# Optimization experiments

Hardware: AMD Instinct MI355X
Metric: run time of the kernel (lower is better)

The kernel has to match this reference:

```python
import jax, jax.numpy as jnp
import numpy as np
from jax import lax

B, S, H, W = 16, 5, 64, 64
D, DS, DEPTH, EXPAND, NC = 128, 16, 2, 2, 2


def _ln(x, w, b, eps=1e-5):
    m = x.mean(-1, keepdims=True)
    v = ((x - m) ** 2).mean(-1, keepdims=True)
    return (x - m) / jnp.sqrt(v + eps) * w + b


def _conv2d(x, w, b, stride, pad):
    y = lax.conv_general_dilated(x, w, (stride, stride), [(pad, pad), (pad, pad)],
                                 dimension_numbers=('NCHW', 'OIHW', 'NCHW'))
    return y + b[None, :, None, None]


def _convT2d(x, w, b):
    # torch ConvTranspose2d(k=4, s=2, p=1); w: (Cin, Cout, 4, 4)
    k = jnp.transpose(w[:, :, ::-1, ::-1], (1, 0, 2, 3))
    y = lax.conv_general_dilated(x, k, (1, 1), [(2, 2), (2, 2)], lhs_dilation=(2, 2),
                                 dimension_numbers=('NCHW', 'OIHW', 'NCHW'))
    return y + b[None, :, None, None]


def _dwconv1d(x, w, b):
    # x: [B, L, D]; torch depthwise Conv1d k=4 pad=3 then truncate to L == left-pad 3
    y = lax.conv_general_dilated(x.transpose(0, 2, 1), w, (1,), [(3, 0)],
                                 feature_group_count=w.shape[0],
                                 dimension_numbers=('NCH', 'OIH', 'NCH'))
    return (y + b[None, :, None]).transpose(0, 2, 1)


def _selective_scan(x, ln_w, ln_b, in_w, in_b, x_w, x_b, A_log, Dm, out_w, out_b):
    xn = _ln(x, ln_w, ln_b)
    xz = xn @ in_w.T + in_b
    xp, z = jnp.split(xz, 2, axis=-1)
    xp = jax.nn.silu(xp)
    z = jax.nn.sigmoid(z)
    u = xp @ x_w.T + x_b                        # [B, L, DS]
    a = jnp.exp(-jnp.exp(A_log))[0, 0]          # [DS] decay factor exp(A), A = -exp(A_log)

    def step(h, u_t):
        h = a * h + u_t
        return h, h

    _, hs = lax.scan(step, jnp.zeros((x.shape[0], DS), x.dtype), u.transpose(1, 0, 2))
    hs = hs.transpose(1, 0, 2)                  # [B, L, DS]
    y = (hs @ Dm) * z
    y = y @ out_w.T + out_b                     # dropout is identity at inference
    return x + y


def setup_inputs() -> dict:
    key = jax.random.key(0)
    ks = iter(jax.random.split(key, 64))

    def nrm(shape, scale=0.02):
        return (jax.random.normal(next(ks), shape) * scale).astype(jnp.float32)

    d, ds, hw = D, DS, H * W
    return {
        'x': jax.random.normal(next(ks), (B, S, H, W), dtype=jnp.float32),
        'emb_w': nrm((d, 1, 3, 3), 0.1), 'emb_b': jnp.zeros((d,), jnp.float32),
        'pos_embed': nrm((hw, d)), 'time_embed': nrm((S, d)),
        'blk_ln1_w': jnp.ones((DEPTH, d), jnp.float32), 'blk_ln1_b': jnp.zeros((DEPTH, d), jnp.float32),
        'blk_conv_w': nrm((DEPTH, d, 1, 4), 0.2), 'blk_conv_b': jnp.zeros((DEPTH, d), jnp.float32),
        'blk_sln_w': jnp.ones((DEPTH, d), jnp.float32), 'blk_sln_b': jnp.zeros((DEPTH, d), jnp.float32),
        'blk_A_log': nrm((DEPTH, 1, 1, ds), 0.5),
        'blk_D': nrm((DEPTH, ds, d), 0.1),
        'blk_in_w': nrm((DEPTH, 2 * d, d), 0.05), 'blk_in_b': jnp.zeros((DEPTH, 2 * d), jnp.float32),
        'blk_x_w': nrm((DEPTH, ds, d), 0.05), 'blk_x_b': jnp.zeros((DEPTH, ds), jnp.float32),
        'blk_out_w': nrm((DEPTH, d, d), 0.05), 'blk_out_b': jnp.zeros((DEPTH, d), jnp.float32),
        'blk_ln2_w': jnp.ones((DEPTH, d), jnp.float32), 'blk_ln2_b': jnp.zeros((DEPTH, d), jnp.float32),
        'blk_mlp_w1': nrm((DEPTH, EXPAND * d, d), 0.05), 'blk_mlp_b1': jnp.zeros((DEPTH, EXPAND * d), jnp.float32),
        'blk_mlp_w2': nrm((DEPTH, d, EXPAND * d), 0.05), 'blk_mlp_b2': jnp.zeros((DEPTH, d), jnp.float32),
        'down1_w': nrm((d, d, 3, 3), 0.05), 'down1_b': jnp.zeros((d,), jnp.float32),
        'down2_w': nrm((2 * d, d, 3, 3), 0.05), 'down2_b': jnp.zeros((2 * d,), jnp.float32),
        'bott_w': nrm((2 * d, 2 * d, 3, 3), 0.05), 'bott_b': jnp.zeros((2 * d,), jnp.float32),
        'up1_w': nrm((2 * d, d, 4, 4), 0.05), 'up1_b': jnp.zeros((d,), jnp.float32),
        'up2_w': nrm((2 * d, d, 4, 4), 0.05), 'up2_b': jnp.zeros((d,), jnp.float32),
        'final_w': nrm((NC, 2 * d, 1, 1), 0.05), 'final_b': jnp.zeros((NC,), jnp.float32),
    }


def reference(x, emb_w, emb_b, pos_embed, time_embed,
              blk_ln1_w, blk_ln1_b, blk_conv_w, blk_conv_b,
              blk_sln_w, blk_sln_b, blk_A_log, blk_D,
              blk_in_w, blk_in_b, blk_x_w, blk_x_b, blk_out_w, blk_out_b,
              blk_ln2_w, blk_ln2_b, blk_mlp_w1, blk_mlp_b1, blk_mlp_w2, blk_mlp_b2,
              down1_w, down1_b, down2_w, down2_b, bott_w, bott_b,
              up1_w, up1_b, up2_w, up2_b, final_w, final_b):
    b, s, h, w = x.shape
    # embed all frames at once (linear combination weights: 0.5 each, last frame 1.0)
    e = _conv2d(x.reshape(b * s, 1, h, w), emb_w, emb_b, 1, 1)      # [B*S, D, H, W]
    e = e.reshape(b, s, D, h * w).transpose(0, 1, 3, 2)              # [B, S, HW, D]
    e = e + pos_embed[None, None] + time_embed[:s][None, :, None, :]
    wts = jnp.where(jnp.arange(s) == s - 1, 1.0, 0.5).astype(x.dtype)
    emb = jnp.einsum('bsld,s->bld', e, wts)                          # [B, HW, D]
    for i in range(DEPTH):
        xn = _ln(emb, blk_ln1_w[i], blk_ln1_b[i])
        emb = emb + _dwconv1d(xn, blk_conv_w[i], blk_conv_b[i])
        emb = _selective_scan(emb, blk_sln_w[i], blk_sln_b[i], blk_in_w[i], blk_in_b[i],
                              blk_x_w[i], blk_x_b[i], blk_A_log[i], blk_D[i],
                              blk_out_w[i], blk_out_b[i])
        m = _ln(emb, blk_ln2_w[i], blk_ln2_b[i])
        m = jax.nn.gelu(m @ blk_mlp_w1[i].T + blk_mlp_b1[i], approximate=False)
        emb = emb + (m @ blk_mlp_w2[i].T + blk_mlp_b2[i])
    sp = emb.transpose(0, 2, 1).reshape(b, D, h, w)
    x1 = jax.nn.relu(_conv2d(sp, down1_w, down1_b, 2, 1))
    x2 = jax.nn.relu(_conv2d(x1, down2_w, down2_b, 2, 1))
    x2 = jax.nn.relu(_conv2d(x2, bott_w, bott_b, 1, 1))
    u1 = jax.nn.relu(_convT2d(x2, up1_w, up1_b))
    u1 = jnp.concatenate([u1, x1], axis=1)
    u2 = jax.nn.relu(_convT2d(u1, up2_w, up2_b))
    u2 = jnp.concatenate([u2, sp], axis=1)
    return _conv2d(u2, final_w, final_b, 1, 0)
```

## Files before the change

kernel.cpp:

```cpp
#include <hip/hip_runtime.h>
#include <cmath>

namespace {
constexpr int Bn = 16, Ln = 4096, Dn = 128, DSn = 16;
constexpr int Mtok = Bn * Ln;
constexpr int SLS = 138;
}

typedef short bfx8 __attribute__((ext_vector_type(8)));
typedef float f32x4 __attribute__((ext_vector_type(4)));

static __device__ __forceinline__ ushort f2bf(float f) {
  union { float f; unsigned u; } v; v.f = f;
  unsigned r = v.u + 0x7fff + ((v.u >> 16) & 1);
  return (ushort)(r >> 16);
}
static __device__ __forceinline__ float bf2f(ushort u) {
  union { unsigned u; float f; } v; v.u = ((unsigned)u) << 16;
  return v.f;
}

__global__ void k_prep(const float* __restrict__ inw, const float* __restrict__ outw,
                       const float* __restrict__ m1, const float* __restrict__ m2,
                       const float* __restrict__ xw, const float* __restrict__ cw,
// ... 131 lines not shown
    r8[e] = (short)f2bf((nv[e] - m) * rs * sw[d] + sb[d]);
  }
  *(bfx8*)(xn2 + (size_t)tok * 128 + d0) = r8;
}

__global__ __launch_bounds__(256) void k_gemm_xz(
    const ushort* __restrict__ A, const ushort* __restrict__ W, const float* __restrict__ bias,
    ushort* __restrict__ Zu, const ushort* __restrict__ xw, const float* __restrict__ xb,
    float* __restrict__ UT) {
  __shared__ ushort sl[128 * SLS];
  const int t = threadIdx.x;
  const int l = t & 63, wv = t >> 6;
  const int l15 = l & 15, q = l >> 4;
  const int wm = wv >> 1, wn = wv & 1;
  const int m0 = blockIdx.x * 128 + wm * 64;
  const int n0 = blockIdx.y * 128 + wn * 64;
  f32x4 acc[4][4] = {};
  const ushort* Ab = A + (size_t)(m0 + l15) * 128 + q * 8;
  const ushort* Wb = W + (size_t)(n0 + l15) * 128 + q * 8;
#pragma unroll
  for (int k0 = 0; k0 < 128; k0 += 32) {
    bfx8 a[4], b[4];
#pragma unroll
    for (int mf = 0; mf < 4; mf++) a[mf] = *(const bfx8*)(Ab + (size_t)mf * 16 * 128 + k0);
#pragma unroll
    for (int nf = 0; nf < 4; nf++) b[nf] = *(const bfx8*)(Wb + (size_t)nf * 16 * 128 + k0);
#pragma unroll
    for (int mf = 0; mf < 4; mf++)
#pragma unroll
      for (int nf = 0; nf < 4; nf++)
        acc[mf][nf] = __builtin_amdgcn_mfma_f32_16x16x32_bf16(a[mf], b[nf], acc[mf][nf], 0, 0, 0);
  }
  if (blockIdx.y == 1) {
#pragma unroll
    for (int mf = 0; mf < 4; mf++)
#pragma unroll
      for (int nf = 0; nf < 4; nf++) {
        const int col = n0 + nf * 16 + l15;
        const float bb = bias[col];
#pragma unroll
        for (int r = 0; r < 4; r++) {
          const int row = m0 + mf * 16 + q * 4 + r;
          float v = acc[mf][nf][r] + bb;
          Zu[(size_t)row * 128 + col - 128] = f2bf(1.f / (1.f + expf(-v)));
        }
      }
    return;
  }
#pragma unroll
  for (int mf = 0; mf < 4; mf++)
#pragma unroll
    for (int nf = 0; nf < 4; nf++) {
      const int col = wn * 64 + nf * 16 + l15;
      const float bb = bias[col];
#pragma unroll
      for (int r = 0; r < 4; r++) {
        const int rowl = wm * 64 + mf * 16 + q * 4 + r;
        float v = acc[mf][nf][r] + bb;
        sl[rowl * SLS + col] = f2bf(v / (1.f + expf(-v)));
      }
    }
  __syncthreads();
  f32x4 pu[2] = {};
#pragma unroll
  for (int k0 = 0; k0 < 128; k0 += 32) {
    bfx8 bx_ = *(const bfx8*)(xw + l15 * 128 + k0 + q * 8);
#pragma unroll
    for (int mi = 0; mi < 2; mi++) {
      bfx8 a2 = *(const bfx8*)&sl[(wv * 32 + mi * 16 + l15) * SLS + k0 + q * 8];
      pu[mi] = __builtin_amdgcn_mfma_f32_16x16x32_bf16(a2, bx_, pu[mi], 0, 0, 0);
    }
  }
  const float ub = xb[l15];
#pragma unroll
  for (int mi = 0; mi < 2; mi++)
#pragma unroll
    for (int r = 0; r < 4; r++) {
      int token = blockIdx.x * 128 + wv * 32 + mi * 16 + q * 4 + r;
      int b = token >> 12, ll = token & 4095;
      UT[((size_t)(b * 16 + l15)) * 4096 + ll] = pu[mi][r] + ub;
    }
}

__global__ __launch_bounds__(256) void k_gemm_om(
    const ushort* __restrict__ A, const ushort* __restrict__ W1, const float* __restrict__ b1,
    float* __restrict__ emb, const float* __restrict__ lw, const float* __restrict__ lb,
    const ushort* __restrict__ W2, const float* __restrict__ b2, ushort* __restrict__ MH) {
  __shared__ ushort sl[128 * SLS];
  __shared__ float red[2][128][2];
  const int t = threadIdx.x;
  const int l = t & 63, wv = t >> 6;
  const int l15 = l & 15, q = l >> 4;
  const int wm = wv >> 1, wn = wv & 1;
  const int m0 = blockIdx.x * 128 + wm * 64;
  const int n0 = wn * 64;
  {
    f32x4 acc[4][4] = {};
    const ushort* Ab = A + (size_t)(m0 + l15) * 128 + q * 8;
    const ushort* Wb = W1 + (size_t)(n0 + l15) * 128 + q * 8;
#pragma unroll
    for (int k0 = 0; k0 < 128; k0 += 32) {
      bfx8 a[4], b[4];
#pragma unroll
      for (int mf = 0; mf < 4; mf++) a[mf] = *(const bfx8*)(Ab + (size_t)mf * 16 * 128 + k0);
#pragma unroll
      for (int nf = 0; nf < 4; nf++) b[nf] = *(const bfx8*)(Wb + (size_t)nf * 16 * 128 + k0);
#pragma unroll
      for (int mf = 0; mf < 4; mf++)
#pragma unroll
        for (int nf = 0; nf < 4; nf++)
          acc[mf][nf] = __builtin_amdgcn_mfma_f32_16x16x32_bf16(a[mf], b[nf], acc[mf][nf], 0, 0, 0);
    }
    float sv[4][4], qv[4][4];
#pragma unroll
    for (int mf = 0; mf < 4; mf++)
#pragma unroll
      for (int r = 0; r < 4; r++) { sv[mf][r] = 0.f; qv[mf][r] = 0.f; }
#pragma unroll
    for (int mf = 0; mf < 4; mf++)
#pragma unroll
      for (int nf = 0; nf < 4; nf++) {
        const int col = n0 + nf * 16 + l15;
        const float bb = b1[col];
#pragma unroll
        for (int r = 0; r < 4; r++) {
          const int row = m0 + mf * 16 + q * 4 + r;
          float v = acc[mf][nf][r] + bb + emb[(size_t)row * 128 + col];
          acc[mf][nf][r] = v;
          sv[mf][r] += v; qv[mf][r] += v * v;
        }
      }
#pragma unroll
    for (int mf = 0; mf < 4; mf++)
#pragma unroll
      for (int r = 0; r < 4; r++) {
#pragma unroll
        for (int off = 1; off < 16; off <<= 1) {
          sv[mf][r] += __shfl_xor(sv[mf][r], off);
          qv[mf][r] += __shfl_xor(qv[mf][r], off);
        }
        if (l15 == 0) {
          int rowl = wm * 64 + mf * 16 + q * 4 + r;
          red[0][rowl][wn] = sv[mf][r];
          red[1][rowl][wn] = qv[mf][r];
        }
      }
    __syncthreads();
#pragma unroll
    for (int mf = 0; mf < 4; mf++)
#pragma unroll
      for (int r = 0; r < 4; r++) {
        const int rowl = wm * 64 + mf * 16 + q * 4 + r;
        const int row = blockIdx.x * 128 + rowl;
        float ts = red[0][rowl][0] + red[0][rowl][1];
        float tq = red[1][rowl][0] + red[1][rowl][1];
        float mm = ts * (1.f / 128.f);
        float var = tq * (1.f / 128.f) - mm * mm;
        float rs = rsqrtf(var + 1e-5f);
#pragma unroll
        for (int nf = 0; nf < 4; nf++) {
          const int col = n0 + nf * 16 + l15;
          float v = acc[mf][nf][r];
          emb[(size_t)row * 128 + col] = v;
          sl[rowl * SLS + col] = f2bf((v - mm) * rs * lw[col] + lb[col]);
        }
      }
  }
  __syncthreads();
#pragma unroll
  for (int p = 0; p < 2; p++) {
    f32x4 acc2[2][8] = {};
#pragma unroll
    for (int k0 = 0; k0 < 128; k0 += 32) {
      bfx8 a2[2];
#pragma unroll
      for (int mi = 0; mi < 2; mi++)
        a2[mi] = *(const bfx8*)&sl[(wv * 32 + mi * 16 + l15) * SLS + k0 + q * 8];
#pragma unroll
      for (int nf = 0; nf < 8; nf++) {
        bfx8 b2v = *(const bfx8*)(W2 + (size_t)(p * 128 + nf * 16 + l15) * 128 + k0 + q * 8);
#pragma unroll
        for (int mi = 0; mi < 2; mi++)
          acc2[mi][nf] = __builtin_amdgcn_mfma_f32_16x16x32_bf16(a2[mi], b2v, acc2[mi][nf], 0, 0, 0);
      }
    }
#pragma unroll
    for (int mi = 0; mi < 2; mi++)
#pragma unroll
      for (int nf = 0; nf < 8; nf++) {
        const int col = p * 128 + nf * 16 + l15;
        const float bb = b2[col];
#pragma unroll
        for (int r = 0; r < 4; r++) {
          const int row = blockIdx.x * 128 + wv * 32 + mi * 16 + q * 4 + r;
          float v = acc2[mi][nf][r] + bb;
          MH[(size_t)row * 256 + col] = f2bf(0.5f * v * (1.f + erff(v * 0.7071067811865475f)));
        }
      }
  }
}

template <int MODE, int K>
__global__ __launch_bounds__(256) void k_mgemm(const ushort* __restrict__ A, const ushort* __restrict__ W,
                                               const float* __restrict__ bias, void* __restrict__ out2v,
                                               float* __restrict__ emb,
                                               const float* __restrict__ lw, const float* __restrict__ lb) {
  __shared__ float red[2][128][2];
  const int t = threadIdx.x;
  const int l = t & 63, wv = t >> 6;
  const int l15 = l & 15, q = l >> 4;
  const int wm = wv >> 1, wn = wv & 1;
  const int m0 = blockIdx.x * 128 + wm * 64;
  const int n0 = wn * 64;
  f32x4 acc[4][4] = {};
  const ushort* Ab = A + (size_t)(m0 + l15) * K + q * 8;
  const ushort* Wb = W + (size_t)(n0 + l15) * K + q * 8;
#pragma unroll
  for (int k0 = 0; k0 < K; k0 += 32) {
    bfx8 a[4], b[4];
#pragma unroll
    for (int mf = 0; mf < 4; mf++) a[mf] = *(const bfx8*)(Ab + (size_t)mf * 16 * K + k0);
#pragma unroll
    for (int nf = 0; nf < 4; nf++) b[nf] = *(const bfx8*)(Wb + (size_t)nf * 16 * K + k0);
#pragma unroll
    for (int mf = 0; mf < 4; mf++)
#pragma unroll
      for (int nf = 0; nf < 4; nf++)
        acc[mf][nf] = __builtin_amdgcn_mfma_f32_16x16x32_bf16(a[mf], b[nf], acc[mf][nf], 0, 0, 0);
  }
  float sv[4][4], qv[4][4];
#pragma unroll
  for (int mf = 0; mf < 4; mf++)
#pragma unroll
    for (int r = 0; r < 4; r++) { sv[mf][r] = 0.f; qv[mf][r] = 0.f; }
#pragma unroll
  for (int mf = 0; mf < 4; mf++)
#pragma unroll
    for (int nf = 0; nf < 4; nf++) {
      const int col = n0 + nf * 16 + l15;
      const float bb = bias[col];
#pragma unroll
      for (int r = 0; r < 4; r++) {
        const int row = m0 + mf * 16 + q * 4 + r;
        float v = acc[mf][nf][r] + bb + emb[(size_t)row * 128 + col];
        acc[mf][nf][r] = v;
        sv[mf][r] += v; qv[mf][r] += v * v;
      }
    }
  if constexpr (MODE == 5) {
#pragma unroll
    for (int mf = 0; mf < 4; mf++)
#pragma unroll
      for (int r = 0; r < 4; r++) {
#pragma unroll
        for (int off = 1; off < 16; off <<= 1) {
          sv[mf][r] += __shfl_xor(sv[mf][r], off);
          qv[mf][r] += __shfl_xor(qv[mf][r], off);
        }
        if (l15 == 0) {
          int rowl = wm * 64 + mf * 16 + q * 4 + r;
          red[0][rowl][wn] = sv[mf][r];
          red[1][rowl][wn] = qv[mf][r];
        }
      }
    __syncthreads();
  }
#pragma unroll
  for (int mf = 0; mf < 4; mf++)
#pragma unroll
    for (int r = 0; r < 4; r++) {
      const int rowl = wm * 64 + mf * 16 + q * 4 + r;
      const int row = blockIdx.x * 128 + rowl;
      float mm = 0.f, rs = 0.f;
      if constexpr (MODE == 5) {
        float ts = red[0][rowl][0] + red[0][rowl][1];
        float tq = red[1][rowl][0] + red[1][rowl][1];
        mm = ts * (1.f / 128.f);
        float var = tq * (1.f / 128.f) - mm * mm;
        rs = rsqrtf(var + 1e-5f);
      }
#pragma unroll
      for (int nf = 0; nf < 4; nf++) {
        const int col = n0 + nf * 16 + l15;
        float v = acc[mf][nf][r];
        emb[(size_t)row * 128 + col] = v;
        if constexpr (MODE == 5)
          ((ushort*)out2v)[(size_t)row * 128 + col] = f2bf((v - mm) * rs * lw[col] + lb[col]);
        else
          ((ushort*)out2v)[(size_t)row * 256 + 128 + col] = f2bf(v);
      }
    }
}

__global__ __launch_bounds__(64) void k_scan(const float* __restrict__ UT, float* __restrict__ HST,
                                             const float* __restrict__ A_log) {
  const int b = blockIdx.x >> 4, ds = blockIdx.x & 15;
  const int tid = threadIdx.x;
  const float a = expf(-expf(A_log[ds]));
  const float4* ut4 = (const float4*)(UT + ((size_t)(b * 16 + ds)) * 4096 + tid * 64);
  float r[64];
#pragma unroll
  for (int j4 = 0; j4 < 16; j4++) {
    float4 v = ut4[j4];
    r[j4 * 4 + 0] = v.x; r[j4 * 4 + 1] = v.y; r[j4 * 4 + 2] = v.z; r[j4 * 4 + 3] = v.w;
  }
  float h = 0.f;
#pragma unroll
  for (int j = 0; j < 64; j++) { h = a * h + r[j]; r[j] = h; }
  float a64 = a;
#pragma unroll
  for (int qq = 0; qq < 6; qq++) a64 *= a64;
  float Ac = a64, Bc = h;
#pragma unroll
  for (int off = 1; off < 64; off <<= 1) {
    float Ap = __shfl_up(Ac, off);
    float Bp = __shfl_up(Bc, off);
    if (tid >= off) { Bc = Ac * Bp + Bc; Ac = Ac * Ap; }
  }
  float carry = __shfl_up(Bc, 1);
  if (tid == 0) carry = 0.f;
  float p = a;
#pragma unroll
  for (int j = 0; j < 64; j++) { r[j] += p * carry; p *= a; }
  float4* hb4 = (float4*)(HST + ((size_t)(b * 16 + ds)) * 4096 + tid * 64);
#pragma unroll
  for (int j4 = 0; j4 < 16; j4++) {
    float4 v; v.x = r[j4 * 4 + 0]; v.y = r[j4 * 4 + 1]; v.z = r[j4 * 4 + 2]; v.w = r[j4 * 4 + 3];
    hb4[j4] = v;
  }
}

__global__ __launch_bounds__(256) void k_yb(const float* __restrict__ HST, const float* __restrict__ Dm_,
                                            const ushort* __restrict__ Z, ushort* __restrict__ Y) {
  const int m = blockIdx.x * 2 + (threadIdx.x >> 7);
  const int d = threadIdx.x & 127;
  const int b = m >> 12, l = m & 4095;
  const float* hb = HST + (size_t)b * 16 * Ln + l;
  float acc = 0.f;
#pragma unroll
  for (int s = 0; s < 16; s++) acc += hb[(size_t)s * Ln] * Dm_[s * 128 + d];
  const size_t o = (size_t)m * 128 + d;
  Y[o] = f2bf(acc * bf2f(Z[o]));
}

template <int MODE, int OTH, int OTW, int CIN, int WPB>
__global__ __launch_bounds__(WPB * 64) void k_cv(
    const ushort* __restrict__ in, ushort* __restrict__ out,
    const ushort* __restrict__ wt, const float* __restrict__ bias,
    int Hi, int Wi, int CP, int CO, int CPo, int COo, int Cout,
    int nsp, int nspx, long ibs, long obs) {
  constexpr int ITH = (MODE == 1) ? (2 * OTH + 1) : (OTH + 2);
  constexpr int ITW = (MODE == 1) ? (2 * OTW + 1) : (OTW + 2);
  constexpr int NPIX = ITH * ITW;
  constexpr int SPF = OTH * OTW / 16;
  constexpr int NTAPS = (MODE == 2) ? 4 : 9;
  constexpr int NCH = CIN / 32;
  __shared__ __attribute__((aligned(16))) ushort lds[NPIX * 40];
  const int t = threadIdx.x;
  const int w = t >> 6, l = t & 63;
  const int l15 = l & 15, q = l >> 4;
  const int b = blockIdx.z;
  const int py = (MODE == 2) ? ((int)blockIdx.y >> 1) : 0;
  const int px = (MODE == 2) ? ((int)blockIdx.y & 1) : 0;
  const int cb = blockIdx.x / nsp;
  const int spt = blockIdx.x - cb * nsp;
  const int spy = spt / nspx, spx = spt - spy * nspx;
  const int n0 = cb * (16 * WPB) + w * 16;
  const int y0 = spy * OTH, x0 = spx * OTW;
  const int gy0 = (MODE == 1) ? (2 * y0 - 1) : (y0 - 1);
  const int gx0 = (MODE == 1) ? (2 * x0 - 1) : (x0 - 1);
  const ushort* ib = in + (size_t)b * ibs;
  f32x4 acc[SPF] = {};
  int abase[SPF];
#pragma unroll
  for (int af = 0; af < SPF; af++) {
    int p = af * 16 + l15;
    int ty = p / OTW, tx = p % OTW;
    int sy = (MODE == 1) ? (2 * ty) : ty;
    int sx = (MODE == 1) ? (2 * tx) : tx;
    abase[af] = (sy * ITW + sx) * 40 + q * 8;
  }
  for (int c = 0; c < NCH; c++) {
    const int k0 = c * 32;
    __syncthreads();
    for (int idx = t; idx < NPIX * 4; idx += WPB * 64) {
      int pix = idx >> 2, qq = idx & 3;
      int sy = pix / ITW, sx = pix - sy * ITW;
      int gy = gy0 + sy, gx = gx0 + sx;
      bfx8 v = {0, 0, 0, 0, 0, 0, 0, 0};
      if ((unsigned)gy < (unsigned)Hi && (unsigned)gx < (unsigned)Wi)
        v = *(const bfx8*)(ib + (size_t)(gy * Wi + gx) * CP + CO + k0 + qq * 8);
      *(bfx8*)&lds[pix * 40 + qq * 8] = v;
    }
    __syncthreads();
#pragma unroll
    for (int tap = 0; tap < NTAPS; tap++) {
      const int dy = (MODE == 2) ? (tap >> 1) : (tap / 3);
      const int dx = (MODE == 2) ? (tap & 1) : (tap - (tap / 3) * 3);
      const int tapw = (MODE == 2) ? ((3 - py - 2 * dy) * 4 + (3 - px - 2 * dx)) : tap;
      const int toff = (MODE == 2) ? (((py + dy) * ITW + (px + dx)) * 40)
                                   : ((dy * ITW + dx) * 40);
      bfx8 bv = *(const bfx8*)(wt + ((size_t)tapw * Cout + n0 + l15) * CIN + k0 + q * 8);
#pragma unroll
      for (int af = 0; af < SPF; af++) {
        bfx8 av = *(const bfx8*)&lds[abase[af] + toff];
        acc[af] = __builtin_amdgcn_mfma_f32_16x16x32_bf16(av, bv, acc[af], 0, 0, 0);
      }
    }
  }
  const float bb = bias[n0 + l15];
  ushort* ob = out + (size_t)b * obs + COo + n0 + l15;
#pragma unroll
  for (int af = 0; af < SPF; af++) {
#pragma unroll
    for (int r = 0; r < 4; r++) {
      int p = af * 16 + q * 4 + r;
      int ty = p / OTW, tx = p % OTW;
      int oy, ox, Wo;
      if (MODE == 2) { oy = (y0 + ty) * 2 + py; ox = (x0 + tx) * 2 + px; Wo = Wi * 2; }
      else if (MODE == 1) { oy = y0 + ty; ox = x0 + tx; Wo = Wi / 2; }
      else { oy = y0 + ty; ox = x0 + tx; Wo = Wi; }
      ob[(size_t)(oy * Wo + ox) * CPo] = f2bf(fmaxf(acc[af][r] + bb, 0.f));
    }
  }
}

__global__ void k_final2(const ushort* __restrict__ in, const float* __restrict__ w,
                         const float* __restrict__ bias, float* __restrict__ out) {
  int i = blockIdx.x * 256 + threadIdx.x;
  int b = i >> 12, p = i & 4095;
  const ushort* row = in + (size_t)i * 256;
  float a0 = bias[0], a1 = bias[1];
  for (int c = 0; c < 256; c += 4) {
    ushort4 u = *(const ushort4*)(row + c);
    float4 w0 = *(const float4*)(w + c);
    float4 w1 = *(const float4*)(w + 256 + c);
    float f0 = bf2f(u.x), f1 = bf2f(u.y), f2 = bf2f(u.z), f3 = bf2f(u.w);
    a0 += f0 * w0.x + f1 * w0.y + f2 * w0.z + f3 * w0.w;
    a1 += f0 * w1.x + f1 * w1.y + f2 * w1.z + f3 * w1.w;
  }
  out[(size_t)b * 8192 + p] = a0;
  out[(size_t)b * 8192 + 4096 + p] = a1;
}

extern "C" void kernel_launch(void* const* d_in, const int* in_sizes, int n_in,
                              void* d_out, int out_size, void* d_ws, size_t ws_size,
                              hipStream_t stream) {
  (void)in_sizes; (void)n_in; (void)out_size; (void)ws_size;
  const float* x          = (const float*)d_in[0];
  const float* emb_w      = (const float*)d_in[1];
  const float* emb_b      = (const float*)d_in[2];
  const float* pos_embed  = (const float*)d_in[3];
  const float* time_embed = (const float*)d_in[4];
  const float* blk_ln1_w  = (const float*)d_in[5];
  const float* blk_ln1_b  = (const float*)d_in[6];
  const float* blk_conv_w = (const float*)d_in[7];
  const float* blk_conv_b = (const float*)d_in[8];
  const float* blk_sln_w  = (const float*)d_in[9];
  const float* blk_sln_b  = (const float*)d_in[10];
  const float* blk_A_log  = (const float*)d_in[11];
  const float* blk_D      = (const float*)d_in[12];
  const float* blk_in_w   = (const float*)d_in[13];
  const float* blk_in_b   = (const float*)d_in[14];
  const float* blk_x_w    = (const float*)d_in[15];
  const float* blk_x_b    = (const float*)d_in[16];
  const float* blk_out_w  = (const float*)d_in[17];
  const float* blk_out_b  = (const float*)d_in[18];
  const float* blk_ln2_w  = (const float*)d_in[19];
  const float* blk_ln2_b  = (const float*)d_in[20];
  const float* blk_mlp_w1 = (const float*)d_in[21];
  const float* blk_mlp_b1 = (const float*)d_in[22];
  const float* blk_mlp_w2 = (const float*)d_in[23];
  const float* blk_mlp_b2 = (const float*)d_in[24];
  const float* down1_w    = (const float*)d_in[25];
  const float* down1_b    = (const float*)d_in[26];
  const float* down2_w    = (const float*)d_in[27];
  const float* down2_b    = (const float*)d_in[28];
  const float* bott_w     = (const float*)d_in[29];
  const float* bott_b     = (const float*)d_in[30];
  const float* up1_w      = (const float*)d_in[31];
  const float* up1_b      = (const float*)d_in[32];
  const float* up2_w      = (const float*)d_in[33];
  const float* up2_b      = (const float*)d_in[34];
  const float* final_w    = (const float*)d_in[35];
  const float* final_b    = (const float*)d_in[36];

  float* ws = (float*)d_ws;
  constexpr size_t F = 1u << 20;
  float* EMB = ws;
  ushort* XN1 = (ushort*)(ws + 8 * F);
  ushort* XN2 = XN1 + 8 * F;
  ushort* MH  = (ushort*)(ws + 16 * F);
  ushort* Zu  = (ushort*)(ws + 24 * F);
  ushort* W3  = (ushort*)(ws + 28 * F);
  float* Ubuf = ws + 32 * F;
  float* HST  = ws + 33 * F;

  ushort* Wi  = W3;
  ushort* Wo  = W3 + 65536;
  ushort* Wm1 = W3 + 98304;
  ushort* Wm2 = W3 + 163840;
  ushort* Wx  = W3 + 229376;
  ushort* Wd1 = W3 + 233472;
  ushort* Wd2 = W3 + 380928;
  ushort* Wb9 = W3 + 675840;
  ushort* Wu1 = W3 + 1265664;
  ushort* Wu2 = W3 + 1789952;
  float*  CWT = (float*)(W3 + 2314240);

  k_prep<<<9044, 256, 0, stream>>>(blk_in_w, blk_out_w, blk_mlp_w1, blk_mlp_w2, blk_x_w,
                                   blk_conv_w, down1_w, down2_w, bott_w, up1_w, up2_w, W3, CWT);
  k_combine<<<256, 256, 0, stream>>>(x, Ubuf);
  k_embedln<<<8192, 256, 0, stream>>>(Ubuf, emb_w, emb_b, pos_embed, time_embed,
                                      blk_ln1_w, blk_ln1_b, EMB, XN1);

  ushort* U2C = MH;
  for (int i = 0; i < 2; i++) {
    k_fuse1<<<4096, 256, 0, stream>>>(XN1, EMB, XN2, CWT + i * 512, blk_conv_b + i * Dn,
                                      blk_sln_w + i * Dn, blk_sln_b + i * Dn);
    k_gemm_xz<<<dim3(512, 2), 256, 0, stream>>>(XN2, Wi + i * 32768, blk_in_b + i * 256,
                                                Zu, Wx + i * 2048, blk_x_b + i * DSn, Ubuf);
    k_scan<<<256, 64, 0, stream>>>(Ubuf, HST, blk_A_log + i * DSn);
    k_yb<<<32768, 256, 0, stream>>>(HST, blk_D + i * DSn * Dn, Zu, XN2);
    k_gemm_om<<<dim3(512, 1), 256, 0, stream>>>(XN2, Wo + i * 16384, blk_out_b + i * Dn,
                                                EMB, blk_ln2_w + i * Dn, blk_ln2_b + i * Dn,
                                                Wm1 + i * 32768, blk_mlp_b1 + i * 256, MH);
    if (i == 0)
      k_mgemm<5, 256><<<dim3(512, 1), 256, 0, stream>>>(MH, Wm2 + i * 32768, blk_mlp_b2 + i * Dn,
                                                        XN1, EMB, blk_ln1_w + Dn, blk_ln1_b + Dn);
    else
      k_mgemm<4, 256><<<dim3(512, 1), 256, 0, stream>>>(MH, Wm2 + i * 32768, blk_mlp_b2 + i * Dn,
                                                        U2C, EMB, nullptr, nullptr);
  }

  ushort* U1C = XN1;
  ushort* X2b = XN1 + 8388608;
  ushort* X3b = X2b + 1048576;

  k_cv<1, 8, 8, 128, 4><<<dim3(2 * 16, 1, 16), 256, 0, stream>>>(
      U2C, U1C, Wd1, down1_b, 64, 64, 256, 128, 256, 128, 128,
      16, 4, 64L * 64 * 256, 32L * 32 * 256);
  k_cv<1, 8, 8, 128, 2><<<dim3(8 * 4, 1, 16), 128, 0, stream>>>(
      U1C, X2b, Wd2, down2_b, 32, 32, 256, 128, 256, 0, 256,
      4, 2, 32L * 32 * 256, 16L * 16 * 256);
  k_cv<0, 8, 8, 256, 2><<<dim3(8 * 4, 1, 16), 128, 0, stream>>>(
      X2b, X3b, Wb9, bott_b, 16, 16, 256, 0, 256, 0, 256,
      4, 2, 16L * 16 * 256, 16L * 16 * 256);
  k_cv<2, 8, 16, 256, 2><<<dim3(4 * 2, 4, 16), 128, 0, stream>>>(
      X3b, U1C, Wu1, up1_b, 16, 16, 256, 0, 256, 0, 128,
      2, 1, 16L * 16 * 256, 32L * 32 * 256);
  k_cv<2, 16, 16, 256, 4><<<dim3(2 * 4, 4, 16), 256, 0, stream>>>(
      U1C, U2C, Wu2, up2_b, 32, 32, 256, 0, 256, 0, 128,
      4, 2, 32L * 32 * 256, 64L * 64 * 256);

  k_final2<<<256, 256, 0, stream>>>(U2C, final_w, final_b, (float*)d_out);
}
```

Baseline: 503.5 us.

## Fuse out-proj, LN2, MLP up and down GEMMs into one kernel; warp-parallel final conv

Merges the out-projection+LN2+MLP1 kernel with the MLP2 GEMM kernel. The GELU hidden activations are now staged through a second shared-memory tile in two 128-column halves, so the 256-wide MH intermediate is never written to or read back from global memory. The final 1x1 conv changes from one thread per pixel looping over 256 channels to one wavefront per pixel with a shuffle reduction, which gives more parallelism and coalesced loads. In exchange, shared memory per block roughly doubles and register pressure rises, which may reduce occupancy.

```diff
diff --git a/kernel.cpp b/kernel.cpp
--- a/kernel.cpp
+++ b/kernel.cpp
@@ -237,11 +237,15 @@
     }
 }
 
-__global__ __launch_bounds__(256) void k_gemm_om(
+template <int MODE>
+__global__ __launch_bounds__(256) void k_blk2(
     const ushort* __restrict__ A, const ushort* __restrict__ W1, const float* __restrict__ b1,
     float* __restrict__ emb, const float* __restrict__ lw, const float* __restrict__ lb,
-    const ushort* __restrict__ W2, const float* __restrict__ b2, ushort* __restrict__ MH) {
-  __shared__ ushort sl[128 * SLS];
+    const ushort* __restrict__ W2, const float* __restrict__ b2,
+    const ushort* __restrict__ W3m, const float* __restrict__ b3,
+    void* __restrict__ out2v, const float* __restrict__ lwn, const float* __restrict__ lbn) {
+  __shared__ ushort sl1[128 * SLS];
+  __shared__ ushort sl2[128 * SLS];
   __shared__ float red[2][128][2];
   const int t = threadIdx.x;
   const int l = t & 63, wv = t >> 6;
@@ -317,71 +321,102 @@
           const int col = n0 + nf * 16 + l15;
           float v = acc[mf][nf][r];
           emb[(size_t)row * 128 + col] = v;
-          sl[rowl * SLS + col] = f2bf((v - mm) * rs * lw[col] + lb[col]);
+          sl1[rowl * SLS + col] = f2bf((v - mm) * rs * lw[col] + lb[col]);
         }
       }
   }
   __syncthreads();
-#pragma unroll
-  for (int p = 0; p < 2; p++) {
-    f32x4 acc2[2][8] = {};
+  {
+    f32x4 g[2][8] = {};
 #pragma unroll
     for (int k0 = 0; k0 < 128; k0 += 32) {
       bfx8 a2[2];
 #pragma unroll
       for (int mi = 0; mi < 2; mi++)
-        a2[mi] = *(const bfx8*)&sl[(wv * 32 + mi * 16 + l15) * SLS + k0 + q * 8];
+        a2[mi] = *(const bfx8*)&sl1[(wv * 32 + mi * 16 + l15) * SLS + k0 + q * 8];
 #pragma unroll
       for (int nf = 0; nf < 8; nf++) {
-        bfx8 b2v = *(const bfx8*)(W2 + (size_t)(p * 128 + nf * 16 + l15) * 128 + k0 + q * 8);
+        bfx8 bv = *(const bfx8*)(W2 + (size_t)(nf * 16 + l15) * 128 + k0 + q * 8);
 #pragma unroll
         for (int mi = 0; mi < 2; mi++)
-          acc2[mi][nf] = __builtin_amdgcn_mfma_f32_16x16x32_bf16(a2[mi], b2v, acc2[mi][nf], 0, 0, 0);
+          g[mi][nf] = __builtin_amdgcn_mfma_f32_16x16x32_bf16(a2[mi], bv, g[mi][nf], 0, 0, 0);
       }
     }
 #pragma unroll
     for (int mi = 0; mi < 2; mi++)
 #pragma unroll
       for (int nf = 0; nf < 8; nf++) {
-        const int col = p * 128 + nf * 16 + l15;
+        const int col = nf * 16 + l15;
         const float bb = b2[col];
 #pragma unroll
         for (int r = 0; r < 4; r++) {
-          const int row = blockIdx.x * 128 + wv * 32 + mi * 16 + q * 4 + r;
-          float v = acc2[mi][nf][r] + bb;
-          MH[(size_t)row * 256 + col] = f2bf(0.5f * v * (1.f + erff(v * 0.7071067811865475f)));
-        }
-      }
-  }
-}
-
-template <int MODE, int K>
-__global__ __launch_bounds__(256) void k_mgemm(const ushort* __restrict__ A, const ushort* __restrict__ W,
-                                               const float* __restrict__ bias, void* __restrict__ out2v,
-                                               float* __restrict__ emb,
-                                               const float* __restrict__ lw, const float* __restrict__ lb) {
-  __shared__ float red[2][128][2];
-  const int t = threadIdx.x;
-  const int l = t & 63, wv = t >> 6;
-  const int l15 = l & 15, q = l >> 4;
-  const int wm = wv >> 1, wn = wv & 1;
-  const int m0 = blockIdx.x * 128 + wm * 64;
-  const int n0 = wn * 64;
-  f32x4 acc[4][4] = {};
-  const ushort* Ab = A + (size_t)(m0 + l15) * K + q * 8;
-  const ushort* Wb = W + (size_t)(n0 + l15) * K + q * 8;
-#pragma unroll
-  for (int k0 = 0; k0 < K; k0 += 32) {
+          const int rowl = wv * 32 + mi * 16 + q * 4 + r;
+          float v = g[mi][nf][r] + bb;
+          sl2[rowl * SLS + col] = f2bf(0.5f * v * (1.f + erff(v * 0.7071067811865475f)));
+        }
+      }
+  }
+  __syncthreads();
+  f32x4 g1[2][8] = {};
+#pragma unroll
+  for (int k0 = 0; k0 < 128; k0 += 32) {
+    bfx8 a2[2];
+#pragma unroll
+    for (int mi = 0; mi < 2; mi++)
+      a2[mi] = *(const bfx8*)&sl1[(wv * 32 + mi * 16 + l15) * SLS + k0 + q * 8];
+#pragma unroll
+    for (int nf = 0; nf < 8; nf++) {
+      bfx8 bv = *(const bfx8*)(W2 + (size_t)(128 + nf * 16 + l15) * 128 + k0 + q * 8);
+#pragma unroll
+      for (int mi = 0; mi < 2; mi++)
+        g1[mi][nf] = __builtin_amdgcn_mfma_f32_16x16x32_bf16(a2[mi], bv, g1[mi][nf], 0, 0, 0);
+    }
+  }
+  f32x4 acc3[4][4] = {};
+#pragma unroll
+  for (int k0 = 0; k0 < 128; k0 += 32) {
     bfx8 a[4], b[4];
 #pragma unroll
-    for (int mf = 0; mf < 4; mf++) a[mf] = *(const bfx8*)(Ab + (size_t)mf * 16 * K + k0);
-#pragma unroll
-    for (int nf = 0; nf < 4; nf++) b[nf] = *(const bfx8*)(Wb + (size_t)nf * 16 * K + k0);
+    for (int mf = 0; mf < 4; mf++)
+      a[mf] = *(const bfx8*)&sl2[(wm * 64 + mf * 16 + l15) * SLS + k0 + q * 8];
+#pragma unroll
+    for (int nf = 0; nf < 4; nf++)
+      b[nf] = *(const bfx8*)(W3m + (size_t)(n0 + nf * 16 + l15) * 256 + k0 + q * 8);
 #pragma unroll
     for (int mf = 0; mf < 4; mf++)
 #pragma unroll
       for (int nf = 0; nf < 4; nf++)
-        acc[mf][nf] = __builtin_amdgcn_mfma_f32_16x16x32_bf16(a[mf], b[nf], acc[mf][nf], 0, 0, 0);
+        acc3[mf][nf] = __builtin_amdgcn_mfma_f32_16x16x32_bf16(a[mf], b[nf], acc3[mf][nf], 0, 0, 0);
+  }
+  __syncthreads();
+#pragma unroll
+  for (int mi = 0; mi < 2; mi++)
+#pragma unroll
+    for (int nf = 0; nf < 8; nf++) {
+      const int col = nf * 16 + l15;
+      const float bb = b2[128 + col];
+#pragma unroll
+      for (int r = 0; r < 4; r++) {
+        const int rowl = wv * 32 + mi * 16 + q * 4 + r;
+        float v = g1[mi][nf][r] + bb;
+        sl2[rowl * SLS + col] = f2bf(0.5f * v * (1.f + erff(v * 0.7071067811865475f)));
+      }
+    }
+  __syncthreads();
+#pragma unroll
+  for (int k0 = 0; k0 < 128; k0 += 32) {
+    bfx8 a[4], b[4];
+#pragma unroll
+    for (int mf = 0; mf < 4; mf++)
+      a[mf] = *(const bfx8*)&sl2[(wm * 64 + mf * 16 + l15) * SLS + k0 + q * 8];
+#pragma unroll
+    for (int nf = 0; nf < 4; nf++)
+      b[nf] = *(const bfx8*)(W3m + (size_t)(n0 + nf * 16 + l15) * 256 + 128 + k0 + q * 8);
+#pragma unroll
+    for (int mf = 0; mf < 4; mf++)
+#pragma unroll
+      for (int nf = 0; nf < 4; nf++)
+        acc3[mf][nf] = __builtin_amdgcn_mfma_f32_16x16x32_bf16(a[mf], b[nf], acc3[mf][nf], 0, 0, 0);
   }
   float sv[4][4], qv[4][4];
 #pragma unroll
@@ -393,12 +428,12 @@
 #pragma unroll
     for (int nf = 0; nf < 4; nf++) {
       const int col = n0 + nf * 16 + l15;
-      const float bb = bias[col];
+      const float bb = b3[col];
 #pragma unroll
       for (int r = 0; r < 4; r++) {
         const int row = m0 + mf * 16 + q * 4 + r;
-        float v = acc[mf][nf][r] + bb + emb[(size_t)row * 128 + col];
-        acc[mf][nf][r] = v;
+        float v = acc3[mf][nf][r] + bb + emb[(size_t)row * 128 + col];
+        acc3[mf][nf][r] = v;
         sv[mf][r] += v; qv[mf][r] += v * v;
       }
     }
@@ -437,12 +472,13 @@
 #pragma unroll
       for (int nf = 0; nf < 4; nf++) {
         const int col = n0 + nf * 16 + l15;
-        float v = acc[mf][nf][r];
-        emb[(size_t)row * 128 + col] = v;
-        if constexpr (MODE == 5)
-          ((ushort*)out2v)[(size_t)row * 128 + col] = f2bf((v - mm) * rs * lw[col] + lb[col]);
-        else
+        float v = acc3[mf][nf][r];
+        if constexpr (MODE == 5) {
+          emb[(size_t)row * 128 + col] = v;
+          ((ushort*)out2v)[(size_t)row * 128 + col] = f2bf((v - mm) * rs * lwn[col] + lbn[col]);
+        } else {
           ((ushort*)out2v)[(size_t)row * 256 + 128 + col] = f2bf(v);
+        }
       }
     }
 }
@@ -580,22 +616,24 @@
   }
 }
 
-__global__ void k_final2(const ushort* __restrict__ in, const float* __restrict__ w,
-                         const float* __restrict__ bias, float* __restrict__ out) {
-  int i = blockIdx.x * 256 + threadIdx.x;
-  int b = i >> 12, p = i & 4095;
-  const ushort* row = in + (size_t)i * 256;
-  float a0 = bias[0], a1 = bias[1];
-  for (int c = 0; c < 256; c += 4) {
-    ushort4 u = *(const ushort4*)(row + c);
-    float4 w0 = *(const float4*)(w + c);
-    float4 w1 = *(const float4*)(w + 256 + c);
-    float f0 = bf2f(u.x), f1 = bf2f(u.y), f2 = bf2f(u.z), f3 = bf2f(u.w);
-    a0 += f0 * w0.x + f1 * w0.y + f2 * w0.z + f3 * w0.w;
-    a1 += f0 * w1.x + f1 * w1.y + f2 * w1.z + f3 * w1.w;
-  }
-  out[(size_t)b * 8192 + p] = a0;
-  out[(size_t)b * 8192 + 4096 + p] = a1;
+__global__ __launch_bounds__(256) void k_final3(const ushort* __restrict__ in, const float* __restrict__ w,
+                                                const float* __restrict__ bias, float* __restrict__ out) {
+  int wid = (blockIdx.x << 2) + (threadIdx.x >> 6);
+  int lane = threadIdx.x & 63;
+  const ushort* rp = in + (size_t)wid * 256 + lane * 4;
+  ushort4 u = *(const ushort4*)rp;
+  float f0 = bf2f(u.x), f1 = bf2f(u.y), f2 = bf2f(u.z), f3 = bf2f(u.w);
+  float4 w0 = *(const float4*)(w + lane * 4);
+  float4 w1 = *(const float4*)(w + 256 + lane * 4);
+  float a0 = f0 * w0.x + f1 * w0.y + f2 * w0.z + f3 * w0.w;
+  float a1 = f0 * w1.x + f1 * w1.y + f2 * w1.z + f3 * w1.w;
+#pragma unroll
+  for (int off = 32; off; off >>= 1) { a0 += __shfl_xor(a0, off); a1 += __shfl_xor(a1, off); }
+  if (lane == 0) {
+    int b = wid >> 12, p = wid & 4095;
+    out[(size_t)b * 8192 + p] = a0 + bias[0];
+    out[(size_t)b * 8192 + 4096 + p] = a1 + bias[1];
+  }
 }
 
 extern "C" void kernel_launch(void* const* d_in, const int* in_sizes, int n_in,
@@ -645,7 +683,7 @@
   float* EMB = ws;
   ushort* XN1 = (ushort*)(ws + 8 * F);
   ushort* XN2 = XN1 + 8 * F;
-  ushort* MH  = (ushort*)(ws + 16 * F);
+  ushort* U2C = (ushort*)(ws + 16 * F);
   ushort* Zu  = (ushort*)(ws + 24 * F);
   ushort* W3  = (ushort*)(ws + 28 * F);
   float* Ubuf = ws + 32 * F;
@@ -669,7 +707,6 @@
   k_embedln<<<8192, 256, 0, stream>>>(Ubuf, emb_w, emb_b, pos_embed, time_embed,
                                       blk_ln1_w, blk_ln1_b, EMB, XN1);
 
-  ushort* U2C = MH;
   for (int i = 0; i < 2; i++) {
     k_fuse1<<<4096, 256, 0, stream>>>(XN1, EMB, XN2, CWT + i * 512, blk_conv_b + i * Dn,
                                       blk_sln_w + i * Dn, blk_sln_b + i * Dn);
@@ -677,15 +714,18 @@
                                                 Zu, Wx + i * 2048, blk_x_b + i * DSn, Ubuf);
     k_scan<<<256, 64, 0, stream>>>(Ubuf, HST, blk_A_log + i * DSn);
     k_yb<<<32768, 256, 0, stream>>>(HST, blk_D + i * DSn * Dn, Zu, XN2);
-    k_gemm_om<<<dim3(512, 1), 256, 0, stream>>>(XN2, Wo + i * 16384, blk_out_b + i * Dn,
-                                                EMB, blk_ln2_w + i * Dn, blk_ln2_b + i * Dn,
-                                                Wm1 + i * 32768, blk_mlp_b1 + i * 256, MH);
     if (i == 0)
-      k_mgemm<5, 256><<<dim3(512, 1), 256, 0, stream>>>(MH, Wm2 + i * 32768, blk_mlp_b2 + i * Dn,
-                                                        XN1, EMB, blk_ln1_w + Dn, blk_ln1_b + Dn);
+      k_blk2<5><<<512, 256, 0, stream>>>(XN2, Wo + i * 16384, blk_out_b + i * Dn,
+                                         EMB, blk_ln2_w + i * Dn, blk_ln2_b + i * Dn,
+                                         Wm1 + i * 32768, blk_mlp_b1 + i * 256,
+                                         Wm2 + i * 32768, blk_mlp_b2 + i * Dn,
+                                         XN1, blk_ln1_w + Dn, blk_ln1_b + Dn);
     else
-      k_mgemm<4, 256><<<dim3(512, 1), 256, 0, stream>>>(MH, Wm2 + i * 32768, blk_mlp_b2 + i * Dn,
-                                                        U2C, EMB, nullptr, nullptr);
+      k_blk2<4><<<512, 256, 0, stream>>>(XN2, Wo + i * 16384, blk_out_b + i * Dn,
+                                         EMB, blk_ln2_w + i * Dn, blk_ln2_b + i * Dn,
+                                         Wm1 + i * 32768, blk_mlp_b1 + i * 256,
+                                         Wm2 + i * 32768, blk_mlp_b2 + i * Dn,
+                                         U2C, nullptr, nullptr);
   }
 
   ushort* U1C = XN1;
@@ -708,5 +748,5 @@
       U1C, U2C, Wu2, up2_b, 32, 32, 256, 0, 256, 0, 128,
       4, 2, 32L * 32 * 256, 64L * 64 * 256);
 
-  k_final2<<<256, 256, 0, stream>>>(U2C, final_w, final_b, (float*)d_out);
-}
+  k_final3<<<16384, 256, 0, stream>>>(U2C, final_w, final_b, (float*)d_out);
+}
```

Result: slower. 529.3 us (+5.1%).

## Halve GEMM row tiles to double grid and parallelize final 1x1 conv per wave

Applied to the files above, without the earlier changes.

The fused out-proj/LN/MLP1 kernel and the MLP2 kernel now process 64 token rows per block instead of 128. Each wave holds half the accumulators and the launch uses twice as many blocks, which raises occupancy and gives better spread across CUs on 65536 tokens. The final 1x1 conv now assigns one wavefront per pixel with a shuffle reduction, replacing one thread per pixel that walked 256 channels serially. The cost is that each weight tile is reloaded by twice as many blocks, and an extra barrier is added in the MODE 4 path.

```diff
diff --git a/kernel.cpp b/kernel.cpp
--- a/kernel.cpp
+++ b/kernel.cpp
@@ -241,52 +241,52 @@
     const ushort* __restrict__ A, const ushort* __restrict__ W1, const float* __restrict__ b1,
     float* __restrict__ emb, const float* __restrict__ lw, const float* __restrict__ lb,
     const ushort* __restrict__ W2, const float* __restrict__ b2, ushort* __restrict__ MH) {
-  __shared__ ushort sl[128 * SLS];
-  __shared__ float red[2][128][2];
+  __shared__ ushort sl1[64 * SLS];
+  __shared__ float red[2][64][2];
   const int t = threadIdx.x;
   const int l = t & 63, wv = t >> 6;
   const int l15 = l & 15, q = l >> 4;
   const int wm = wv >> 1, wn = wv & 1;
-  const int m0 = blockIdx.x * 128 + wm * 64;
+  const int m0 = blockIdx.x * 64;
   const int n0 = wn * 64;
   {
-    f32x4 acc[4][4] = {};
-    const ushort* Ab = A + (size_t)(m0 + l15) * 128 + q * 8;
+    f32x4 acc[2][4] = {};
+    const ushort* Ab = A + (size_t)(m0 + wm * 32 + l15) * 128 + q * 8;
     const ushort* Wb = W1 + (size_t)(n0 + l15) * 128 + q * 8;
 #pragma unroll
     for (int k0 = 0; k0 < 128; k0 += 32) {
-      bfx8 a[4], b[4];
-#pragma unroll
-      for (int mf = 0; mf < 4; mf++) a[mf] = *(const bfx8*)(Ab + (size_t)mf * 16 * 128 + k0);
+      bfx8 a[2], b[4];
+#pragma unroll
+      for (int mf = 0; mf < 2; mf++) a[mf] = *(const bfx8*)(Ab + (size_t)mf * 16 * 128 + k0);
 #pragma unroll
       for (int nf = 0; nf < 4; nf++) b[nf] = *(const bfx8*)(Wb + (size_t)nf * 16 * 128 + k0);
 #pragma unroll
-      for (int mf = 0; mf < 4; mf++)
+      for (int mf = 0; mf < 2; mf++)
 #pragma unroll
         for (int nf = 0; nf < 4; nf++)
           acc[mf][nf] = __builtin_amdgcn_mfma_f32_16x16x32_bf16(a[mf], b[nf], acc[mf][nf], 0, 0, 0);
     }
-    float sv[4][4], qv[4][4];
-#pragma unroll
-    for (int mf = 0; mf < 4; mf++)
+    float sv[2][4], qv[2][4];
+#pragma unroll
+    for (int mf = 0; mf < 2; mf++)
 #pragma unroll
       for (int r = 0; r < 4; r++) { sv[mf][r] = 0.f; qv[mf][r] = 0.f; }
 #pragma unroll
-    for (int mf = 0; mf < 4; mf++)
+    for (int mf = 0; mf < 2; mf++)
 #pragma unroll
       for (int nf = 0; nf < 4; nf++) {
         const int col = n0 + nf * 16 + l15;
         const float bb = b1[col];
 #pragma unroll
         for (int r = 0; r < 4; r++) {
-          const int row = m0 + mf * 16 + q * 4 + r;
+          const int row = m0 + wm * 32 + mf * 16 + q * 4 + r;
           float v = acc[mf][nf][r] + bb + emb[(size_t)row * 128 + col];
           acc[mf][nf][r] = v;
           sv[mf][r] += v; qv[mf][r] += v * v;
         }
       }
 #pragma unroll
-    for (int mf = 0; mf < 4; mf++)
+    for (int mf = 0; mf < 2; mf++)
 #pragma unroll
       for (int r = 0; r < 4; r++) {
 #pragma unroll
@@ -295,18 +295,18 @@
           qv[mf][r] += __shfl_xor(qv[mf][r], off);
         }
         if (l15 == 0) {
-          int rowl = wm * 64 + mf * 16 + q * 4 + r;
+          int rowl = wm * 32 + mf * 16 + q * 4 + r;
           red[0][rowl][wn] = sv[mf][r];
           red[1][rowl][wn] = qv[mf][r];
         }
       }
     __syncthreads();
 #pragma unroll
-    for (int mf = 0; mf < 4; mf++)
+    for (int mf = 0; mf < 2; mf++)
 #pragma unroll
       for (int r = 0; r < 4; r++) {
-        const int rowl = wm * 64 + mf * 16 + q * 4 + r;
-        const int row = blockIdx.x * 128 + rowl;
+        const int rowl = wm * 32 + mf * 16 + q * 4 + r;
+        const int row = m0 + rowl;
         float ts = red[0][rowl][0] + red[0][rowl][1];
         float tq = red[1][rowl][0] + red[1][rowl][1];
         float mm = ts * (1.f / 128.f);
@@ -317,42 +317,41 @@
           const int col = n0 + nf * 16 + l15;
           float v = acc[mf][nf][r];
           emb[(size_t)row * 128 + col] = v;
-          sl[rowl * SLS + col] = f2bf((v - mm) * rs * lw[col] + lb[col]);
+          sl1[rowl * SLS + col] = f2bf((v - mm) * rs * lw[col] + lb[col]);
         }
       }
   }
   __syncthreads();
-#pragma unroll
-  for (int p = 0; p < 2; p++) {
-    f32x4 acc2[2][8] = {};
-#pragma unroll
-    for (int k0 = 0; k0 < 128; k0 += 32) {
-      bfx8 a2[2];
+  const int rw0 = (wv & 1) * 32;
+  const int cw0 = (wv >> 1) * 128;
+  f32x4 acc2[2][8] = {};
+#pragma unroll
+  for (int k0 = 0; k0 < 128; k0 += 32) {
+    bfx8 a2[2];
+#pragma unroll
+    for (int mi = 0; mi < 2; mi++)
+      a2[mi] = *(const bfx8*)&sl1[(rw0 + mi * 16 + l15) * SLS + k0 + q * 8];
+#pragma unroll
+    for (int nf = 0; nf < 8; nf++) {
+      bfx8 b2v = *(const bfx8*)(W2 + (size_t)(cw0 + nf * 16 + l15) * 128 + k0 + q * 8);
 #pragma unroll
       for (int mi = 0; mi < 2; mi++)
-        a2[mi] = *(const bfx8*)&sl[(wv * 32 + mi * 16 + l15) * SLS + k0 + q * 8];
-#pragma unroll
-      for (int nf = 0; nf < 8; nf++) {
-        bfx8 b2v = *(const bfx8*)(W2 + (size_t)(p * 128 + nf * 16 + l15) * 128 + k0 + q * 8);
-#pragma unroll
-        for (int mi = 0; mi < 2; mi++)
-          acc2[mi][nf] = __builtin_amdgcn_mfma_f32_16x16x32_bf16(a2[mi], b2v, acc2[mi][nf], 0, 0, 0);
-      }
-    }
-#pragma unroll
-    for (int mi = 0; mi < 2; mi++)
-#pragma unroll
-      for (int nf = 0; nf < 8; nf++) {
-        const int col = p * 128 + nf * 16 + l15;
-        const float bb = b2[col];
-#pragma unroll
-        for (int r = 0; r < 4; r++) {
-          const int row = blockIdx.x * 128 + wv * 32 + mi * 16 + q * 4 + r;
-          float v = acc2[mi][nf][r] + bb;
-          MH[(size_t)row * 256 + col] = f2bf(0.5f * v * (1.f + erff(v * 0.7071067811865475f)));
-        }
-      }
-  }
+        acc2[mi][nf] = __builtin_amdgcn_mfma_f32_16x16x32_bf16(a2[mi], b2v, acc2[mi][nf], 0, 0, 0);
+    }
+  }
+#pragma unroll
+  for (int mi = 0; mi < 2; mi++)
+#pragma unroll
+    for (int nf = 0; nf < 8; nf++) {
+      const int col = cw0 + nf * 16 + l15;
+      const float bb = b2[col];
+#pragma unroll
+      for (int r = 0; r < 4; r++) {
+        const int row = m0 + rw0 + mi * 16 + q * 4 + r;
+        float v = acc2[mi][nf][r] + bb;
+        MH[(size_t)row * 256 + col] = f2bf(0.5f * v * (1.f + erff(v * 0.7071067811865475f)));
+      }
+    }
 }
 
 template <int MODE, int K>
@@ -360,43 +359,44 @@
                                                const float* __restrict__ bias, void* __restrict__ out2v,
                                                float* __restrict__ emb,
                                                const float* __restrict__ lw, const float* __restrict__ lb) {
-  __shared__ float red[2][128][2];
+  __shared__ float red[2][64][2];
   const int t = threadIdx.x;
   const int l = t & 63, wv = t >> 6;
   const int l15 = l & 15, q = l >> 4;
   const int wm = wv >> 1, wn = wv & 1;
-  const int m0 = blockIdx.x * 128 + wm * 64;
+  const int m0 = blockIdx.x * 64;
   const int n0 = wn * 64;
-  f32x4 acc[4][4] = {};
-  const ushort* Ab = A + (size_t)(m0 + l15) * K + q * 8;
+  f32x4 acc[2][4] = {};
+  const ushort* Ab = A + (size_t)(m0 + wm * 32 + l15) * K + q * 8;
   const ushort* Wb = W + (size_t)(n0 + l15) * K + q * 8;
 #pragma unroll
   for (int k0 = 0; k0 < K; k0 += 32) {
-    bfx8 a[4], b[4];
-#pragma unroll
-    for (int mf = 0; mf < 4; mf++) a[mf] = *(const bfx8*)(Ab + (size_t)mf * 16 * K + k0);
+    bfx8 a[2], b[4];
+#pragma unroll
+    for (int mf = 0; mf < 2; mf++) a[mf] = *(const bfx8*)(Ab + (size_t)mf * 16 * K + k0);
 #pragma unroll
     for (int nf = 0; nf < 4; nf++) b[nf] = *(const bfx8*)(Wb + (size_t)nf * 16 * K + k0);
 #pragma unroll
-    for (int mf = 0; mf < 4; mf++)
+    for (int mf = 0; mf < 2; mf++)
 #pragma unroll
       for (int nf = 0; nf < 4; nf++)
         acc[mf][nf] = __builtin_amdgcn_mfma_f32_16x16x32_bf16(a[mf], b[nf], acc[mf][nf], 0, 0, 0);
   }
-  float sv[4][4], qv[4][4];
-#pragma unroll
-  for (int mf = 0; mf < 4; mf++)
+  if constexpr (MODE == 4) __syncthreads();
+  float sv[2][4], qv[2][4];
+#pragma unroll
+  for (int mf = 0; mf < 2; mf++)
 #pragma unroll
     for (int r = 0; r < 4; r++) { sv[mf][r] = 0.f; qv[mf][r] = 0.f; }
 #pragma unroll
-  for (int mf = 0; mf < 4; mf++)
+  for (int mf = 0; mf < 2; mf++)
 #pragma unroll
     for (int nf = 0; nf < 4; nf++) {
       const int col = n0 + nf * 16 + l15;
       const float bb = bias[col];
 #pragma unroll
       for (int r = 0; r < 4; r++) {
-        const int row = m0 + mf * 16 + q * 4 + r;
+        const int row = m0 + wm * 32 + mf * 16 + q * 4 + r;
         float v = acc[mf][nf][r] + bb + emb[(size_t)row * 128 + col];
         acc[mf][nf][r] = v;
         sv[mf][r] += v; qv[mf][r] += v * v;
@@ -404,7 +404,7 @@
     }
   if constexpr (MODE == 5) {
 #pragma unroll
-    for (int mf = 0; mf < 4; mf++)
+    for (int mf = 0; mf < 2; mf++)
 #pragma unroll
       for (int r = 0; r < 4; r++) {
 #pragma unroll
@@ -413,7 +413,7 @@
           qv[mf][r] += __shfl_xor(qv[mf][r], off);
         }
         if (l15 == 0) {
-          int rowl = wm * 64 + mf * 16 + q * 4 + r;
+          int rowl = wm * 32 + mf * 16 + q * 4 + r;
           red[0][rowl][wn] = sv[mf][r];
           red[1][rowl][wn] = qv[mf][r];
         }
@@ -421,11 +421,11 @@
     __syncthreads();
   }
 #pragma unroll
-  for (int mf = 0; mf < 4; mf++)
+  for (int mf = 0; mf < 2; mf++)
 #pragma unroll
     for (int r = 0; r < 4; r++) {
-      const int rowl = wm * 64 + mf * 16 + q * 4 + r;
-      const int row = blockIdx.x * 128 + rowl;
+      const int rowl = wm * 32 + mf * 16 + q * 4 + r;
+      const int row = m0 + rowl;
       float mm = 0.f, rs = 0.f;
       if constexpr (MODE == 5) {
         float ts = red[0][rowl][0] + red[0][rowl][1];
@@ -580,22 +580,24 @@
   }
 }
 
-__global__ void k_final2(const ushort* __restrict__ in, const float* __restrict__ w,
-                         const float* __restrict__ bias, float* __restrict__ out) {
-  int i = blockIdx.x * 256 + threadIdx.x;
-  int b = i >> 12, p = i & 4095;
-  const ushort* row = in + (size_t)i * 256;
-  float a0 = bias[0], a1 = bias[1];
-  for (int c = 0; c < 256; c += 4) {
-    ushort4 u = *(const ushort4*)(row + c);
-    float4 w0 = *(const float4*)(w + c);
-    float4 w1 = *(const float4*)(w + 256 + c);
-    float f0 = bf2f(u.x), f1 = bf2f(u.y), f2 = bf2f(u.z), f3 = bf2f(u.w);
-    a0 += f0 * w0.x + f1 * w0.y + f2 * w0.z + f3 * w0.w;
-    a1 += f0 * w1.x + f1 * w1.y + f2 * w1.z + f3 * w1.w;
-  }
-  out[(size_t)b * 8192 + p] = a0;
-  out[(size_t)b * 8192 + 4096 + p] = a1;
+__global__ __launch_bounds__(256) void k_final3(const ushort* __restrict__ in, const float* __restrict__ w,
+                                                const float* __restrict__ bias, float* __restrict__ out) {
+  int wid = (blockIdx.x << 2) + (threadIdx.x >> 6);
+  int lane = threadIdx.x & 63;
+  const ushort* rp = in + (size_t)wid * 256 + lane * 4;
+  ushort4 u = *(const ushort4*)rp;
+  float f0 = bf2f(u.x), f1 = bf2f(u.y), f2 = bf2f(u.z), f3 = bf2f(u.w);
+  float4 w0 = *(const float4*)(w + lane * 4);
+  float4 w1 = *(const float4*)(w + 256 + lane * 4);
+  float a0 = f0 * w0.x + f1 * w0.y + f2 * w0.z + f3 * w0.w;
+  float a1 = f0 * w1.x + f1 * w1.y + f2 * w1.z + f3 * w1.w;
+#pragma unroll
+  for (int off = 32; off; off >>= 1) { a0 += __shfl_xor(a0, off); a1 += __shfl_xor(a1, off); }
+  if (lane == 0) {
+    int b = wid >> 12, p = wid & 4095;
+    out[(size_t)b * 8192 + p] = a0 + bias[0];
+    out[(size_t)b * 8192 + 4096 + p] = a1 + bias[1];
+  }
 }
 
 extern "C" void kernel_launch(void* const* d_in, const int* in_sizes, int n_in,
@@ -677,15 +679,15 @@
                                                 Zu, Wx + i * 2048, blk_x_b + i * DSn, Ubuf);
     k_scan<<<256, 64, 0, stream>>>(Ubuf, HST, blk_A_log + i * DSn);
     k_yb<<<32768, 256, 0, stream>>>(HST, blk_D + i * DSn * Dn, Zu, XN2);
-    k_gemm_om<<<dim3(512, 1), 256, 0, stream>>>(XN2, Wo + i * 16384, blk_out_b + i * Dn,
-                                                EMB, blk_ln2_w + i * Dn, blk_ln2_b + i * Dn,
-                                                Wm1 + i * 32768, blk_mlp_b1 + i * 256, MH);
+    k_gemm_om<<<1024, 256, 0, stream>>>(XN2, Wo + i * 16384, blk_out_b + i * Dn,
+                                        EMB, blk_ln2_w + i * Dn, blk_ln2_b + i * Dn,
+                                        Wm1 + i * 32768, blk_mlp_b1 + i * 256, MH);
     if (i == 0)
-      k_mgemm<5, 256><<<dim3(512, 1), 256, 0, stream>>>(MH, Wm2 + i * 32768, blk_mlp_b2 + i * Dn,
-                                                        XN1, EMB, blk_ln1_w + Dn, blk_ln1_b + Dn);
+      k_mgemm<5, 256><<<1024, 256, 0, stream>>>(MH, Wm2 + i * 32768, blk_mlp_b2 + i * Dn,
+                                                XN1, EMB, blk_ln1_w + Dn, blk_ln1_b + Dn);
     else
-      k_mgemm<4, 256><<<dim3(512, 1), 256, 0, stream>>>(MH, Wm2 + i * 32768, blk_mlp_b2 + i * Dn,
-                                                        U2C, EMB, nullptr, nullptr);
+      k_mgemm<4, 256><<<1024, 256, 0, stream>>>(MH, Wm2 + i * 32768, blk_mlp_b2 + i * Dn,
+                                                U2C, EMB, nullptr, nullptr);
   }
 
   ushort* U1C = XN1;
@@ -708,5 +710,5 @@
       U1C, U2C, Wu2, up2_b, 32, 32, 256, 0, 256, 0, 128,
       4, 2, 32L * 32 * 256, 64L * 64 * 256);
 
-  k_final2<<<256, 256, 0, stream>>>(U2C, final_w, final_b, (float*)d_out);
-}
+  k_final3<<<16384, 256, 0, stream>>>(U2C, final_w, final_b, (float*)d_out);
+}
```

New measurement: 523.0 us. 1.04x slower.
